# Optimization experiments

Hardware: AMD Instinct MI355X
Metric: run time of the kernel (lower is better)

## Reference

```python
import jax, jax.numpy as jnp
import numpy as np

MODES = 256


def setup_inputs() -> dict:
    key = jax.random.key(0)
    k1, k2, k3, k4, k5 = jax.random.split(key, 5)
    B, C_IN, C_OUT, N, KM = 8, 128, 128, 8192, 32
    scale = 1.0 / (C_IN * C_OUT)
    return {
        "x": jax.random.normal(k1, (B, C_IN, N), dtype=jnp.float32),
        "wbases": jax.random.normal(k2, (B, N, MODES), dtype=jnp.float32),
        "bases": jax.random.normal(k3, (B, N, MODES), dtype=jnp.float32),
        "weights": scale * jax.random.normal(k4, (C_IN, C_OUT, KM), dtype=jnp.float32),
        "D": jax.random.normal(k5, (KM, MODES), dtype=jnp.float32),
    }


def reference(x, wbases, bases, weights, D):
    # Project onto weighted bases: (b, c_in, n) x (b, n, modes) -> (b, c_in, modes)
    x_hat = jnp.einsum('bcx,bxk->bck', x, wbases[:, :, :MODES])
    # D-weighted channel mixing. Original: x_hat1[b,i,j,k] = x_hat[b,i,k]*D[j,k];
    # y[b,o,k] = sum_{i,j} x_hat1[b,i,j,k] * weights[i,o,j]
    # Equivalent fused contraction (same math, no 4D broadcast):
    y_hat = jnp.einsum('bik,jk,ioj->bok', x_hat, D, weights)
    # Reconstruct on output bases: (b, c_out, modes) x (b, n, modes) -> (b, c_out, n)
    y = jnp.einsum('bck,bxk->bcx', y_hat, bases[:, :, :MODES])
    return y
```

## Files before the change

kernel.cpp:

```cpp
#include <hip/hip_runtime.h>

#define B_    8
#define CIN   128
#define COUT  128
#define NX    8192
#define KMJ   32
#define MODES 256

typedef short bf16x8 __attribute__((ext_vector_type(8)));
typedef float f32x4  __attribute__((ext_vector_type(4)));

__device__ __forceinline__ float bf2f(unsigned short u) {
    union { unsigned int i; float f; } v; v.i = ((unsigned int)u) << 16; return v.f;
}
__device__ __forceinline__ unsigned short f2bf(float f) {
    union { float f; unsigned int i; } v; v.f = f;
    unsigned int x = v.i;
    return (unsigned short)((x + 0x7fffu + ((x >> 16) & 1u)) >> 16);
}
__device__ __forceinline__ bf16x8 cvt8(const float* __restrict__ p) {
    f32x4 a = *(const f32x4*)p;
    f32x4 b = *(const f32x4*)(p + 4);
    bf16x8 r;
    r[0] = (short)f2bf(a[0]); r[1] = (short)f2bf(a[1]);
    r[2] = (short)f2bf(a[2]); r[3] = (short)f2bf(a[3]);
    r[4] = (short)f2bf(b[0]); r[5] = (short)f2bf(b[1]);
    r[6] = (short)f2bf(b[2]); r[7] = (short)f2bf(b[3]);
    return r;
}

__global__ __launch_bounds__(256) void k1_wk(const float* __restrict__ W,
                                             const float* __restrict__ D,
                                             unsigned short* __restrict__ Wk) {
    int wave = threadIdx.x >> 6;
    int lane = threadIdx.x & 63;
    int gw   = blockIdx.x * 4 + wave;
    int kt   = gw & 15;
    int ioch = gw >> 4;
    int k0   = kt * 16;
    int quad = lane >> 4, l16 = lane & 15;

    bf16x8 bfrag;
#pragma unroll
    for (int jj = 0; jj < 8; jj++)
        bfrag[jj] = (short)f2bf(D[(quad * 8 + jj) * MODES + k0 + l16]);

    int io0 = ioch * 256;
#pragma unroll 4
    for (int t = 0; t < 16; t++) {
        int io = io0 + t * 16 + l16;
        bf16x8 afrag = cvt8(W + (size_t)io * KMJ + quad * 8);
        f32x4 acc = {0.f, 0.f, 0.f, 0.f};
        acc = __builtin_amdgcn_mfma_f32_16x16x32_bf16(afrag, bfrag, acc, 0, 0, 0);
        int iorow = io0 + t * 16 + quad * 4;
        ushort4 st;
        st.x = f2bf(acc[0]); st.y = f2bf(acc[1]);
        st.z = f2bf(acc[2]); st.w = f2bf(acc[3]);
        *(ushort4*)(Wk + (size_t)(k0 + l16) * (CIN * COUT) + iorow) = st;
    }
}

__global__ __launch_bounds__(512) void k2_xhat(const float* __restrict__ X,
                                               const float* __restrict__ WB,
                                               float* __restrict__ XH) {
    int b = blockIdx.y;
    int r0 = blockIdx.x * 256;
    int wave = threadIdx.x >> 6;
    int lane = threadIdx.x & 63;
    int wm = wave >> 2;
    int wn = wave & 3;
    int quad = lane >> 4, l16 = lane & 15;

    const float* xb  = X  + (size_t)b * CIN * NX;
    const float* wbb = WB + (size_t)b * NX * MODES;

    f32x4 acc[4][4];
#pragma unroll
    for (int i = 0; i < 4; i++)
#pragma unroll
        for (int j = 0; j < 4; j++) acc[i][j] = (f32x4){0.f, 0.f, 0.f, 0.f};

    for (int step = 0; step < 8; step++) {
        int rs = r0 + step * 32;
        bf16x8 af[4];
#pragma unroll
        for (int tm = 0; tm < 4; tm++) {
            int c = wm * 64 + tm * 16 + l16;
            af[tm] = cvt8(xb + (size_t)c * NX + rs + quad * 8);
        }
        bf16x8 bfv[4];
#pragma unroll
        for (int tn = 0; tn < 4; tn++) {
            int km = wn * 64 + tn * 16 + l16;
            const float* p = wbb + (size_t)(rs + quad * 8) * MODES + km;
#pragma unroll
            for (int jj = 0; jj < 8; jj++) bfv[tn][jj] = (short)f2bf(p[jj * MODES]);
        }
#pragma unroll
        for (int tm = 0; tm < 4; tm++)
#pragma unroll
            for (int tn = 0; tn < 4; tn++)
                acc[tm][tn] = __builtin_amdgcn_mfma_f32_16x16x32_bf16(af[tm], bfv[tn], acc[tm][tn], 0, 0, 0);
    }

    float* xhb = XH + (size_t)b * CIN * MODES;
#pragma unroll
    for (int tm = 0; tm < 4; tm++) {
        int c = wm * 64 + tm * 16 + quad * 4;
#pragma unroll
        for (int tn = 0; tn < 4; tn++) {
            int km = wn * 64 + tn * 16 + l16;
#pragma unroll
            for (int r = 0; r < 4; r++)
                atomicAdd(xhb + (size_t)(c + r) * MODES + km, acc[tm][tn][r]);
        }
    }
}

__global__ __launch_bounds__(256) void k3_yhat(const float* __restrict__ XH,
                                               const unsigned short* __restrict__ Wk,
                                               unsigned short* __restrict__ YH) {
    __shared__ float xs[8][128];
    __shared__ float ys[8][128];
    int b  = blockIdx.y;
    int k0 = blockIdx.x * 8;
    int t  = threadIdx.x;
    const float* xhb = XH + (size_t)b * CIN * MODES;
#pragma unroll
    for (int l = 0; l < 4; l++) {
        int e = l * 256 + t;
        int kk = e & 7, i = e >> 3;
        xs[kk][i] = xhb[(size_t)i * MODES + k0 + kk];
    }
    __syncthreads();
    int o = t & 127, kh = t >> 7;
#pragma unroll
    for (int p = 0; p < 4; p++) {
        int kk = p * 2 + kh;
        int k  = k0 + kk;
        const unsigned short* wp = Wk + (size_t)k * (CIN * COUT) + o;
        float acc = 0.f;
#pragma unroll 8
        for (int i = 0; i < 128; i++)
            acc += xs[kk][i] * bf2f(wp[i * COUT]);
        ys[kk][o] = acc;
    }
    __syncthreads();
    unsigned short* yb = YH + (size_t)b * COUT * MODES;
#pragma unroll
    for (int l = 0; l < 4; l++) {
        int e = l * 256 + t;
        int kk = e & 7, oo = e >> 3;
        yb[(size_t)oo * MODES + k0 + kk] = f2bf(ys[kk][oo]);
    }
}

__global__ __launch_bounds__(256) void k4_y(const unsigned short* __restrict__ YH,
                                            const float* __restrict__ BA,
                                            float* __restrict__ Y) {
    __shared__ __align__(16) unsigned short As[128 * 32];
    __shared__ __align__(16) unsigned short Bs[128 * 32];
    int b  = blockIdx.y;
    int n0 = blockIdx.x * 128;
    int t  = threadIdx.x;
    int wave = t >> 6, lane = t & 63;
    int wm = wave >> 1, wn = wave & 1;
    int quad = lane >> 4, l16 = lane & 15;

    const unsigned short* yhb = YH + (size_t)b * COUT * MODES;
    const float* bab = BA + (size_t)b * NX * MODES + (size_t)n0 * MODES;

    f32x4 acc[4][4];
#pragma unroll
    for (int i = 0; i < 4; i++)
#pragma unroll
        for (int j = 0; j < 4; j++) acc[i][j] = (f32x4){0.f, 0.f, 0.f, 0.f};

    for (int step = 0; step < 8; step++) {
        int ks = step * 32;
#pragma unroll
        for (int p = 0; p < 2; p++) {
            int E = p * 2048 + t * 8;
            int row = E >> 5, kk = E & 31;
            bf16x8 av = *(const bf16x8*)(yhb + (size_t)row * MODES + ks + kk);
            bf16x8 bv = cvt8(bab + (size_t)row * MODES + ks + kk);
            *(bf16x8*)(As + E) = av;
            *(bf16x8*)(Bs + E) = bv;
        }
        __syncthreads();

        bf16x8 af[4], bfv[4];
#pragma unroll
        for (int tm = 0; tm < 4; tm++) {
            int c = wm * 64 + tm * 16 + l16;
            af[tm] = *(const bf16x8*)(As + c * 32 + quad * 8);
        }
#pragma unroll
        for (int tn = 0; tn < 4; tn++) {
            int n = wn * 64 + tn * 16 + l16;
            bfv[tn] = *(const bf16x8*)(Bs + n * 32 + quad * 8);
        }
#pragma unroll
        for (int tm = 0; tm < 4; tm++)
#pragma unroll
            for (int tn = 0; tn < 4; tn++)
                acc[tm][tn] = __builtin_amdgcn_mfma_f32_16x16x32_bf16(af[tm], bfv[tn], acc[tm][tn], 0, 0, 0);
        __syncthreads();
    }

    float* yb = Y + (size_t)b * COUT * NX;
#pragma unroll
    for (int tm = 0; tm < 4; tm++) {
        int o = wm * 64 + tm * 16 + quad * 4;
#pragma unroll
        for (int tn = 0; tn < 4; tn++) {
            int n = n0 + wn * 64 + tn * 16 + l16;
#pragma unroll
            for (int r = 0; r < 4; r++)
                yb[(size_t)(o + r) * NX + n] = acc[tm][tn][r];
        }
    }
}

extern "C" void kernel_launch(void* const* d_in, const int* in_sizes, int n_in,
                              void* d_out, int out_size, void* d_ws, size_t ws_size,
                              hipStream_t stream) {
    const float* X  = (const float*)d_in[0];
    const float* WB = (const float*)d_in[1];
    const float* BA = (const float*)d_in[2];
    const float* W  = (const float*)d_in[3];
    const float* D  = (const float*)d_in[4];
    float* Y = (float*)d_out;

    char* ws = (char*)d_ws;
    float*          XH = (float*)ws;
    unsigned short* Wk = (unsigned short*)(ws + (1u << 20));
    unsigned short* YH = (unsigned short*)(ws + (1u << 20) + (size_t)CIN * COUT * MODES * 2);

    hipMemsetAsync(XH, 0, (size_t)B_ * CIN * MODES * sizeof(float), stream);

    k1_wk  <<<256,        256, 0, stream>>>(W, D, Wk);
    k2_xhat<<<dim3(32, 8), 512, 0, stream>>>(X, WB, XH);
    k3_yhat<<<dim3(32, 8), 256, 0, stream>>>(XH, Wk, YH);
    k4_y   <<<dim3(64, 8), 256, 0, stream>>>(YH, BA, Y);
}
```

Measured before the change: 251.4 us.

## Stage k2 inputs through LDS with coalesced vector loads and split modes

The x-hat projection kernel now loads X and wbases tiles with coalesced float4 global reads, converts them to bf16 and stores them in padded shared memory. MFMA fragments are then read from LDS, replacing the strided scalar global loads of wbases that the old kernel used. The grid also gains a mode-split dimension (two halves of 128 modes) with 256-thread blocks, which doubles the block count. This adds two barriers per step and some LDS bank-conflict risk on the column-wise B-fragment reads.

```diff
diff --git a/kernel.cpp b/kernel.cpp
--- a/kernel.cpp
+++ b/kernel.cpp
@@ -26,6 +26,11 @@
     r[2] = (short)f2bf(a[2]); r[3] = (short)f2bf(a[3]);
     r[4] = (short)f2bf(b[0]); r[5] = (short)f2bf(b[1]);
     r[6] = (short)f2bf(b[2]); r[7] = (short)f2bf(b[3]);
+    return r;
+}
+__device__ __forceinline__ ushort4 cvt4(f32x4 a) {
+    ushort4 r;
+    r.x = f2bf(a[0]); r.y = f2bf(a[1]); r.z = f2bf(a[2]); r.w = f2bf(a[3]);
     return r;
 }
 
@@ -60,19 +65,25 @@
     }
 }
 
-__global__ __launch_bounds__(512) void k2_xhat(const float* __restrict__ X,
+__global__ __launch_bounds__(256) void k2_xhat(const float* __restrict__ X,
                                                const float* __restrict__ WB,
                                                float* __restrict__ XH) {
-    int b = blockIdx.y;
-    int r0 = blockIdx.x * 256;
-    int wave = threadIdx.x >> 6;
-    int lane = threadIdx.x & 63;
-    int wm = wave >> 2;
-    int wn = wave & 3;
+    __shared__ __align__(16) unsigned short Xs[128 * 40];
+    __shared__ __align__(16) unsigned short WBs[32 * 140];
+    int nt = blockIdx.x;
+    int kt = blockIdx.y;
+    int b  = blockIdx.z;
+    int r0 = nt * 256;
+    int t  = threadIdx.x;
+    int wave = t >> 6, lane = t & 63;
+    int wm = wave >> 1, wn = wave & 1;
     int quad = lane >> 4, l16 = lane & 15;
 
     const float* xb  = X  + (size_t)b * CIN * NX;
-    const float* wbb = WB + (size_t)b * NX * MODES;
+    const float* wbb = WB + (size_t)b * NX * MODES + kt * 128;
+
+    int xn4 = t & 7,  xc0 = t >> 3;
+    int wm4 = t & 31, wn0 = t >> 5;
 
     f32x4 acc[4][4];
 #pragma unroll
@@ -80,21 +91,38 @@
 #pragma unroll
         for (int j = 0; j < 4; j++) acc[i][j] = (f32x4){0.f, 0.f, 0.f, 0.f};
 
-    for (int step = 0; step < 8; step++) {
-        int rs = r0 + step * 32;
+    for (int s = 0; s < 8; s++) {
+        int rs = r0 + s * 32;
+        f32x4 xv[4], wv[4];
+#pragma unroll
+        for (int r = 0; r < 4; r++)
+            xv[r] = *(const f32x4*)(xb + (size_t)(xc0 + 32 * r) * NX + rs + xn4 * 4);
+#pragma unroll
+        for (int r = 0; r < 4; r++)
+            wv[r] = *(const f32x4*)(wbb + (size_t)(rs + wn0 + 8 * r) * MODES + wm4 * 4);
+
+        __syncthreads();
+#pragma unroll
+        for (int r = 0; r < 4; r++)
+            *(ushort4*)(Xs + (xc0 + 32 * r) * 40 + xn4 * 4) = cvt4(xv[r]);
+#pragma unroll
+        for (int r = 0; r < 4; r++)
+            *(ushort4*)(WBs + (wn0 + 8 * r) * 140 + wm4 * 4) = cvt4(wv[r]);
+        __syncthreads();
+
         bf16x8 af[4];
 #pragma unroll
         for (int tm = 0; tm < 4; tm++) {
             int c = wm * 64 + tm * 16 + l16;
-            af[tm] = cvt8(xb + (size_t)c * NX + rs + quad * 8);
+            af[tm] = *(const bf16x8*)(Xs + c * 40 + quad * 8);
         }
         bf16x8 bfv[4];
 #pragma unroll
         for (int tn = 0; tn < 4; tn++) {
             int km = wn * 64 + tn * 16 + l16;
-            const float* p = wbb + (size_t)(rs + quad * 8) * MODES + km;
-#pragma unroll
-            for (int jj = 0; jj < 8; jj++) bfv[tn][jj] = (short)f2bf(p[jj * MODES]);
+#pragma unroll
+            for (int jj = 0; jj < 8; jj++)
+                bfv[tn][jj] = (short)WBs[(quad * 8 + jj) * 140 + km];
         }
 #pragma unroll
         for (int tm = 0; tm < 4; tm++)
@@ -103,7 +131,7 @@
                 acc[tm][tn] = __builtin_amdgcn_mfma_f32_16x16x32_bf16(af[tm], bfv[tn], acc[tm][tn], 0, 0, 0);
     }
 
-    float* xhb = XH + (size_t)b * CIN * MODES;
+    float* xhb = XH + (size_t)b * CIN * MODES + kt * 128;
 #pragma unroll
     for (int tm = 0; tm < 4; tm++) {
         int c = wm * 64 + tm * 16 + quad * 4;
@@ -239,8 +267,8 @@
 
     hipMemsetAsync(XH, 0, (size_t)B_ * CIN * MODES * sizeof(float), stream);
 
-    k1_wk  <<<256,        256, 0, stream>>>(W, D, Wk);
-    k2_xhat<<<dim3(32, 8), 512, 0, stream>>>(X, WB, XH);
-    k3_yhat<<<dim3(32, 8), 256, 0, stream>>>(XH, Wk, YH);
-    k4_y   <<<dim3(64, 8), 256, 0, stream>>>(YH, BA, Y);
-}
+    k1_wk  <<<256,            256, 0, stream>>>(W, D, Wk);
+    k2_xhat<<<dim3(32, 2, 8), 256, 0, stream>>>(X, WB, XH);
+    k3_yhat<<<dim3(32, 8),    256, 0, stream>>>(XH, Wk, YH);
+    k4_y   <<<dim3(64, 8),    256, 0, stream>>>(YH, BA, Y);
+}
```

After: 251.1 us. About the same (-0.1%).
